# Performance work log

Measured on AMD Instinct MI355X. Metric: run time of the kernel, lower is better.

The kernel has to match this reference:

```python
import jax, jax.numpy as jnp
import numpy as np

B, LQ, LK, NF = 8, 8192, 1024, 64


def setup_inputs() -> dict:
    key = jax.random.key(0)
    k1, k2, k3, k4, k5 = jax.random.split(key, 5)
    x = jax.random.normal(k1, (B, LQ, NF), dtype=jnp.float32)
    kv = jax.random.normal(k2, (B, LK, NF), dtype=jnp.float32)
    # 1x1 submanifold convolutions == per-point linear maps (no bias)
    scale = 1.0 / np.sqrt(NF)
    Wq = jax.random.normal(k3, (NF, NF), dtype=jnp.float32) * scale
    Wk = jax.random.normal(k4, (NF, NF), dtype=jnp.float32) * scale
    Wv = jax.random.normal(k5, (NF, NF), dtype=jnp.float32) * scale
    return {"x": x, "kv": kv, "Wq": Wq, "Wk": Wk, "Wv": Wv}


def reference(x, kv, Wq, Wk, Wv):
    # q/k/v projections (1x1 convs on sparse features = dense matmuls)
    q = jnp.einsum("bqd,de->bqe", x, Wq)    # [B, LQ, NF]
    k = jnp.einsum("bkd,de->bke", kv, Wk)   # [B, LK, NF]
    v = jnp.einsum("bkd,de->bke", kv, Wv)   # [B, LK, NF]
    # per-batch (block-diagonal / ragged) attention: e = q k^T, softmax over keys, @ v
    scores = jnp.einsum("bqe,bke->bqk", q, k)        # [B, LQ, LK] (no scaling, as in source)
    attn = jax.nn.softmax(scores, axis=-1)
    out = jnp.einsum("bqk,bke->bqe", attn, v)        # [B, LQ, NF]
    return out
```

## Files before the change

kernel.cpp:

```cpp
#include <hip/hip_runtime.h>
#include <hip/hip_fp16.h>

constexpr int B_  = 8;
constexpr int LQ  = 8192;
constexpr int LK  = 1024;
constexpr int NF  = 64;
constexpr int PAD = 8;
constexpr int LDW = NF + PAD;

typedef _Float16 f16x8 __attribute__((ext_vector_type(8)));
typedef _Float16 f16x4 __attribute__((ext_vector_type(4)));
typedef float    f32x4 __attribute__((ext_vector_type(4)));

#define MFMA16(a, b, c) __builtin_amdgcn_mfma_f32_16x16x32_f16((a), (b), (c), 0, 0, 0)

__device__ __forceinline__ f16x8 cvt8(const float* p) {
  float4 a = ((const float4*)p)[0];
  float4 b = ((const float4*)p)[1];
  f16x8 r;
  r[0] = (_Float16)a.x; r[1] = (_Float16)a.y; r[2] = (_Float16)a.z; r[3] = (_Float16)a.w;
  r[4] = (_Float16)b.x; r[5] = (_Float16)b.y; r[6] = (_Float16)b.z; r[7] = (_Float16)b.w;
  return r;
}

__device__ __forceinline__ f16x8 ldf(const _Float16* p) { return *(const f16x8*)p; }

__device__ __forceinline__ void st_pk4(_Float16* dst, float a, float b, float c, float d) {
  auto lo = __builtin_amdgcn_cvt_pkrtz(a, b);
  auto hi = __builtin_amdgcn_cvt_pkrtz(c, d);
  auto v  = __builtin_shufflevector(lo, hi, 0, 1, 2, 3);
  *(decltype(v)*)dst = v;
}

__global__ __launch_bounds__(256) void kv_proj_kernel(
    const float* __restrict__ kv, const float* __restrict__ Wk,
    const float* __restrict__ Wv, _Float16* __restrict__ Kb,
    _Float16* __restrict__ Vt) {
  __shared__ __align__(16) _Float16 wkT[NF][LDW];
  __shared__ __align__(16) _Float16 wvT[NF][LDW];
  __shared__ __align__(16) _Float16 ktile[64][LDW];
  __shared__ __align__(16) _Float16 vtileT[64][LDW];

  const int t    = threadIdx.x;
  const int wave = t >> 6, lane = t & 63, g = lane >> 4, c = lane & 15;
  const int b    = blockIdx.x >> 4;
  const int key_base = (blockIdx.x & 15) * 64;

#pragma unroll
  for (int i = 0; i < 16; ++i) {
    int idx = t + 256 * i;
    int e = idx >> 6, d = idx & 63;
    wkT[d][e] = (_Float16)Wk[idx];
    wvT[d][e] = (_Float16)Wv[idx];
  }

  const float* src = kv + ((size_t)b * LK + key_base + wave * 16 + c) * NF;
  f16x8 a0 = cvt8(src + g * 8);
  f16x8 a1 = cvt8(src + 32 + g * 8);
  __syncthreads();

#pragma unroll
  for (int mb = 0; mb < 4; ++mb) {
    f32x4 kacc = {0.f, 0.f, 0.f, 0.f};
    const _Float16* wk0 = &wkT[mb * 16 + c][g * 8];
    kacc = MFMA16(ldf(wk0),      a0, kacc);
    kacc = MFMA16(ldf(wk0 + 32), a1, kacc);
    st_pk4(&ktile[wave * 16 + c][mb * 16 + g * 4], kacc[0], kacc[1], kacc[2], kacc[3]);

    f32x4 vacc = {0.f, 0.f, 0.f, 0.f};
    const _Float16* wv0 = &wvT[mb * 16 + c][g * 8];
    vacc = MFMA16(a0, ldf(wv0),      vacc);
    vacc = MFMA16(a1, ldf(wv0 + 32), vacc);
    st_pk4(&vtileT[mb * 16 + c][wave * 16 + g * 4], vacc[0], vacc[1], vacc[2], vacc[3]);
  }
  __syncthreads();

  const int srow = t >> 2, scol = (t & 3) * 16;
  {
    float4* kd = (float4*)(Kb + ((size_t)b * LK + key_base + srow) * NF + scol);
    kd[0] = *(float4*)&ktile[srow][scol];
    kd[1] = *(float4*)&ktile[srow][scol + 8];
    float4* vd = (float4*)(Vt + ((size_t)b * NF + srow) * LK + key_base + scol);
    vd[0] = *(float4*)&vtileT[srow][scol];
    vd[1] = *(float4*)&vtileT[srow][scol + 8];
  }
}

__global__ __launch_bounds__(256) void attn_kernel(
    const float* __restrict__ x, const float* __restrict__ Wq,
    const _Float16* __restrict__ Kb, const _Float16* __restrict__ Vt,
    float* __restrict__ out) {
  __shared__ __align__(16) _Float16 wqT[NF][LDW];
  __shared__ __align__(16) _Float16 ks[64][LDW];
  __shared__ __align__(16) _Float16 vs[64][LDW];
  __shared__ __align__(16) _Float16 ps[4][16][LDW];

  const int t    = threadIdx.x;
  const int wave = t >> 6, lane = t & 63, g = lane >> 4, c = lane & 15;
  const int b    = blockIdx.x >> 7;
  const int q_base = (blockIdx.x & 127) * 64;
  constexpr float LOG2E = 1.44269504088896f;

#pragma unroll
  for (int i = 0; i < 16; ++i) {
    int idx = t + 256 * i;
    wqT[idx & 63][idx >> 6] = (_Float16)(Wq[idx] * LOG2E);
  }

  const float* xrow = x + ((size_t)b * LQ + q_base + wave * 16 + c) * NF;
  f16x8 xa0 = cvt8(xrow + g * 8);
  f16x8 xa1 = cvt8(xrow + 32 + g * 8);

  const _Float16* Kg = Kb + (size_t)b * LK * NF;
  const _Float16* Vg = Vt + (size_t)b * NF * LK;
  const int srow = t >> 2, scol = (t & 3) * 16;

  float4 kp0, kp1, vp0, vp1;
  {
    const float4* kp = (const float4*)(Kg + (size_t)t * 16);
    kp0 = kp[0]; kp1 = kp[1];
    const float4* vp = (const float4*)(Vg + (size_t)srow * LK + scol);
    vp0 = vp[0]; vp1 = vp[1];
  }
  __syncthreads();

#pragma unroll
  for (int mb = 0; mb < 4; ++mb) {
    f32x4 qacc = {0.f, 0.f, 0.f, 0.f};
    const _Float16* wq0 = &wqT[mb * 16 + c][g * 8];
    qacc = MFMA16(ldf(wq0),      xa0, qacc);
    qacc = MFMA16(ldf(wq0 + 32), xa1, qacc);
    st_pk4(&ps[wave][c][mb * 16 + g * 4], qacc[0], qacc[1], qacc[2], qacc[3]);
  }
  f16x8 qb0 = ldf(&ps[wave][c][g * 8]);
  f16x8 qb1 = ldf(&ps[wave][c][32 + g * 8]);

  float m_s = -1e30f, l_s = 0.f;
  f32x4 oacc[4];
#pragma unroll
  for (int nb = 0; nb < 4; ++nb) oacc[nb] = {0.f, 0.f, 0.f, 0.f};

  for (int tile = 0; tile < 16; ++tile) {
    __syncthreads();
    *(f16x8*)&ks[srow][scol]     = *(f16x8*)&kp0;
    *(f16x8*)&ks[srow][scol + 8] = *(f16x8*)&kp1;
    *(f16x8*)&vs[srow][scol]     = *(f16x8*)&vp0;
    *(f16x8*)&vs[srow][scol + 8] = *(f16x8*)&vp1;
    __syncthreads();
    if (tile < 15) {
      const float4* kp = (const float4*)(Kg + (size_t)(tile + 1) * 64 * NF + t * 16);
      kp0 = kp[0]; kp1 = kp[1];
      const float4* vp = (const float4*)(Vg + (size_t)srow * LK + (tile + 1) * 64 + scol);
      vp0 = vp[0]; vp1 = vp[1];
    }

    f32x4 st[4];
#pragma unroll
    for (int kb = 0; kb < 4; ++kb) {
      st[kb] = {0.f, 0.f, 0.f, 0.f};
      const _Float16* kf = &ks[kb * 16 + c][g * 8];
      st[kb] = MFMA16(ldf(kf),      qb0, st[kb]);
      st[kb] = MFMA16(ldf(kf + 32), qb1, st[kb]);
    }

    float tmax = st[0][0];
#pragma unroll
    for (int kb = 0; kb < 4; ++kb)
#pragma unroll
      for (int r = 0; r < 4; ++r) tmax = fmaxf(tmax, st[kb][r]);
    tmax = fmaxf(tmax, __shfl_xor(tmax, 16));
    tmax = fmaxf(tmax, __shfl_xor(tmax, 32));

    float mnew  = fmaxf(m_s, tmax);
    float alpha = __builtin_amdgcn_exp2f(m_s - mnew);
    m_s = mnew;

    float rsum = 0.f;
#pragma unroll
    for (int kb = 0; kb < 4; ++kb)
#pragma unroll
      for (int r = 0; r < 4; ++r) {
        float p = __builtin_amdgcn_exp2f(st[kb][r] - mnew);
        st[kb][r] = p;
        rsum += p;
      }
    rsum += __shfl_xor(rsum, 16);
    rsum += __shfl_xor(rsum, 32);
    l_s = l_s * alpha + rsum;

    float aq[4];
#pragma unroll
    for (int r = 0; r < 4; ++r) aq[r] = __shfl(alpha, 4 * g + r);
#pragma unroll
    for (int nb = 0; nb < 4; ++nb)
#pragma unroll
      for (int r = 0; r < 4; ++r) oacc[nb][r] *= aq[r];

#pragma unroll
    for (int kb = 0; kb < 4; ++kb)
      st_pk4(&ps[wave][c][kb * 16 + g * 4], st[kb][0], st[kb][1], st[kb][2], st[kb][3]);
    f16x8 pa0 = ldf(&ps[wave][c][g * 8]);
    f16x8 pa1 = ldf(&ps[wave][c][32 + g * 8]);

#pragma unroll
    for (int nb = 0; nb < 4; ++nb) {
      const _Float16* vf = &vs[nb * 16 + c][g * 8];
      oacc[nb] = MFMA16(pa0, ldf(vf),      oacc[nb]);
      oacc[nb] = MFMA16(pa1, ldf(vf + 32), oacc[nb]);
    }
  }

  float linv = 1.0f / l_s;
  float lq[4];
#pragma unroll
  for (int r = 0; r < 4; ++r) lq[r] = __shfl(linv, 4 * g + r);
#pragma unroll
  for (int nb = 0; nb < 4; ++nb)
#pragma unroll
    for (int r = 0; r < 4; ++r)
      out[((size_t)b * LQ + q_base + wave * 16 + g * 4 + r) * NF + nb * 16 + c] =
          oacc[nb][r] * lq[r];
}

extern "C" void kernel_launch(void* const* d_in, const int* in_sizes, int n_in,
                              void* d_out, int out_size, void* d_ws, size_t ws_size,
                              hipStream_t stream) {
  const float* x  = (const float*)d_in[0];
  const float* kv = (const float*)d_in[1];
  const float* Wq = (const float*)d_in[2];
  const float* Wk = (const float*)d_in[3];
  const float* Wv = (const float*)d_in[4];
  float* out = (float*)d_out;

  _Float16* Kb = (_Float16*)d_ws;
  _Float16* Vt = Kb + (size_t)B_ * LK * NF;

  kv_proj_kernel<<<B_ * (LK / 64), 256, 0, stream>>>(kv, Wk, Wv, Kb, Vt);
  attn_kernel<<<B_ * (LQ / 64), 256, 0, stream>>>(x, Wq, Kb, Vt, out);
}
```

Baseline: 114.0 us.

## Process two query sub-tiles per wave and keep softmax probabilities in registers

The attention kernel drops to 128 threads per block, with each wave handling 32 query rows as two 16-row sub-tiles. Each K and V fragment read from LDS now feeds twice as many MFMAs. K and V are stored pre-permuted by the projection kernel, so Q and the probabilities P are packed straight from MFMA accumulators into operand registers, removing the LDS round trip through ps. A ballot skips the output rescale when the running max does not change, and Wq staging reuses the K tile buffer. The cost is higher register pressure from doubled accumulators, V loads that are no longer prefetched, and fewer threads to hide latency.

```diff
diff --git a/kernel.cpp b/kernel.cpp
--- a/kernel.cpp
+++ b/kernel.cpp
@@ -9,7 +9,6 @@
 constexpr int LDW = NF + PAD;
 
 typedef _Float16 f16x8 __attribute__((ext_vector_type(8)));
-typedef _Float16 f16x4 __attribute__((ext_vector_type(4)));
 typedef float    f32x4 __attribute__((ext_vector_type(4)));
 
 #define MFMA16(a, b, c) __builtin_amdgcn_mfma_f32_16x16x32_f16((a), (b), (c), 0, 0, 0)
@@ -30,6 +29,17 @@
   auto hi = __builtin_amdgcn_cvt_pkrtz(c, d);
   auto v  = __builtin_shufflevector(lo, hi, 0, 1, 2, 3);
   *(decltype(v)*)dst = v;
+}
+
+__device__ __forceinline__ f16x8 pack8(f32x4 u, f32x4 v) {
+  auto a = __builtin_amdgcn_cvt_pkrtz(u[0], u[1]);
+  auto b = __builtin_amdgcn_cvt_pkrtz(u[2], u[3]);
+  auto cc = __builtin_amdgcn_cvt_pkrtz(v[0], v[1]);
+  auto d = __builtin_amdgcn_cvt_pkrtz(v[2], v[3]);
+  f16x8 r;
+  r[0] = a[0]; r[1] = a[1]; r[2] = b[0];  r[3] = b[1];
+  r[4] = cc[0]; r[5] = cc[1]; r[6] = d[0]; r[7] = d[1];
+  return r;
 }
 
 __global__ __launch_bounds__(256) void kv_proj_kernel(
@@ -65,13 +75,15 @@
     const _Float16* wk0 = &wkT[mb * 16 + c][g * 8];
     kacc = MFMA16(ldf(wk0),      a0, kacc);
     kacc = MFMA16(ldf(wk0 + 32), a1, kacc);
-    st_pk4(&ktile[wave * 16 + c][mb * 16 + g * 4], kacc[0], kacc[1], kacc[2], kacc[3]);
+    st_pk4(&ktile[wave * 16 + c][(8 * (mb >> 1) + 2 * g + (mb & 1)) * 4],
+           kacc[0], kacc[1], kacc[2], kacc[3]);
 
     f32x4 vacc = {0.f, 0.f, 0.f, 0.f};
     const _Float16* wv0 = &wvT[mb * 16 + c][g * 8];
     vacc = MFMA16(a0, ldf(wv0),      vacc);
     vacc = MFMA16(a1, ldf(wv0 + 32), vacc);
-    st_pk4(&vtileT[mb * 16 + c][wave * 16 + g * 4], vacc[0], vacc[1], vacc[2], vacc[3]);
+    st_pk4(&vtileT[mb * 16 + c][(8 * (wave >> 1) + 2 * g + (wave & 1)) * 4],
+           vacc[0], vacc[1], vacc[2], vacc[3]);
   }
   __syncthreads();
 
@@ -86,14 +98,12 @@
   }
 }
 
-__global__ __launch_bounds__(256) void attn_kernel(
+__global__ __launch_bounds__(128, 4) void attn_kernel(
     const float* __restrict__ x, const float* __restrict__ Wq,
     const _Float16* __restrict__ Kb, const _Float16* __restrict__ Vt,
     float* __restrict__ out) {
-  __shared__ __align__(16) _Float16 wqT[NF][LDW];
   __shared__ __align__(16) _Float16 ks[64][LDW];
   __shared__ __align__(16) _Float16 vs[64][LDW];
-  __shared__ __align__(16) _Float16 ps[4][16][LDW];
 
   const int t    = threadIdx.x;
   const int wave = t >> 6, lane = t & 63, g = lane >> 4, c = lane & 15;
@@ -102,124 +112,147 @@
   constexpr float LOG2E = 1.44269504088896f;
 
 #pragma unroll
-  for (int i = 0; i < 16; ++i) {
-    int idx = t + 256 * i;
-    wqT[idx & 63][idx >> 6] = (_Float16)(Wq[idx] * LOG2E);
-  }
-
-  const float* xrow = x + ((size_t)b * LQ + q_base + wave * 16 + c) * NF;
-  f16x8 xa0 = cvt8(xrow + g * 8);
-  f16x8 xa1 = cvt8(xrow + 32 + g * 8);
+  for (int i = 0; i < 32; ++i) {
+    int idx = t + 128 * i;
+    ks[idx & 63][idx >> 6] = (_Float16)(Wq[idx] * LOG2E);
+  }
 
   const _Float16* Kg = Kb + (size_t)b * LK * NF;
   const _Float16* Vg = Vt + (size_t)b * NF * LK;
-  const int srow = t >> 2, scol = (t & 3) * 16;
-
-  float4 kp0, kp1, vp0, vp1;
+  const int srow = t >> 1, shalf = t & 1;
+
+  f16x8 kpre[4];
   {
-    const float4* kp = (const float4*)(Kg + (size_t)t * 16);
-    kp0 = kp[0]; kp1 = kp[1];
-    const float4* vp = (const float4*)(Vg + (size_t)srow * LK + scol);
-    vp0 = vp[0]; vp1 = vp[1];
-  }
-  __syncthreads();
-
-#pragma unroll
-  for (int mb = 0; mb < 4; ++mb) {
-    f32x4 qacc = {0.f, 0.f, 0.f, 0.f};
-    const _Float16* wq0 = &wqT[mb * 16 + c][g * 8];
-    qacc = MFMA16(ldf(wq0),      xa0, qacc);
-    qacc = MFMA16(ldf(wq0 + 32), xa1, qacc);
-    st_pk4(&ps[wave][c][mb * 16 + g * 4], qacc[0], qacc[1], qacc[2], qacc[3]);
-  }
-  f16x8 qb0 = ldf(&ps[wave][c][g * 8]);
-  f16x8 qb1 = ldf(&ps[wave][c][32 + g * 8]);
-
-  float m_s = -1e30f, l_s = 0.f;
-  f32x4 oacc[4];
-#pragma unroll
-  for (int nb = 0; nb < 4; ++nb) oacc[nb] = {0.f, 0.f, 0.f, 0.f};
+    const f16x8* kp = (const f16x8*)(Kg + srow * NF + shalf * 32);
+    kpre[0] = kp[0]; kpre[1] = kp[1]; kpre[2] = kp[2]; kpre[3] = kp[3];
+  }
+  __syncthreads();
+
+  f16x8 qb[2][2];
+#pragma unroll
+  for (int s = 0; s < 2; ++s) {
+    const float* xrow = x + ((size_t)b * LQ + q_base + wave * 32 + s * 16 + c) * NF;
+    f16x8 xa0 = cvt8(xrow + g * 8);
+    f16x8 xa1 = cvt8(xrow + 32 + g * 8);
+    f32x4 qa[4];
+#pragma unroll
+    for (int mb = 0; mb < 4; ++mb) {
+      qa[mb] = {0.f, 0.f, 0.f, 0.f};
+      const _Float16* wq0 = &ks[mb * 16 + c][g * 8];
+      qa[mb] = MFMA16(ldf(wq0),      xa0, qa[mb]);
+      qa[mb] = MFMA16(ldf(wq0 + 32), xa1, qa[mb]);
+    }
+    qb[s][0] = pack8(qa[0], qa[1]);
+    qb[s][1] = pack8(qa[2], qa[3]);
+  }
+  __syncthreads();
+
+  float m_s[2] = {-1e30f, -1e30f}, l_s[2] = {0.f, 0.f};
+  f32x4 oacc[2][4];
+#pragma unroll
+  for (int s = 0; s < 2; ++s)
+#pragma unroll
+    for (int nb = 0; nb < 4; ++nb) oacc[s][nb] = {0.f, 0.f, 0.f, 0.f};
 
   for (int tile = 0; tile < 16; ++tile) {
-    __syncthreads();
-    *(f16x8*)&ks[srow][scol]     = *(f16x8*)&kp0;
-    *(f16x8*)&ks[srow][scol + 8] = *(f16x8*)&kp1;
-    *(f16x8*)&vs[srow][scol]     = *(f16x8*)&vp0;
-    *(f16x8*)&vs[srow][scol + 8] = *(f16x8*)&vp1;
+    *(f16x8*)&ks[srow][shalf * 32]      = kpre[0];
+    *(f16x8*)&ks[srow][shalf * 32 + 8]  = kpre[1];
+    *(f16x8*)&ks[srow][shalf * 32 + 16] = kpre[2];
+    *(f16x8*)&ks[srow][shalf * 32 + 24] = kpre[3];
+    {
+      const f16x8* vp = (const f16x8*)(Vg + (size_t)srow * LK + tile * 64 + shalf * 32);
+      f16x8 v0 = vp[0], v1 = vp[1], v2 = vp[2], v3 = vp[3];
+      *(f16x8*)&vs[srow][shalf * 32]      = v0;
+      *(f16x8*)&vs[srow][shalf * 32 + 8]  = v1;
+      *(f16x8*)&vs[srow][shalf * 32 + 16] = v2;
+      *(f16x8*)&vs[srow][shalf * 32 + 24] = v3;
+    }
     __syncthreads();
     if (tile < 15) {
-      const float4* kp = (const float4*)(Kg + (size_t)(tile + 1) * 64 * NF + t * 16);
-      kp0 = kp[0]; kp1 = kp[1];
-      const float4* vp = (const float4*)(Vg + (size_t)srow * LK + (tile + 1) * 64 + scol);
-      vp0 = vp[0]; vp1 = vp[1];
-    }
-
-    f32x4 st[4];
+      const f16x8* kp = (const f16x8*)(Kg + (size_t)(tile + 1) * 64 * NF + srow * NF + shalf * 32);
+      kpre[0] = kp[0]; kpre[1] = kp[1]; kpre[2] = kp[2]; kpre[3] = kp[3];
+    }
+
+    f32x4 st[2][4];
 #pragma unroll
     for (int kb = 0; kb < 4; ++kb) {
-      st[kb] = {0.f, 0.f, 0.f, 0.f};
       const _Float16* kf = &ks[kb * 16 + c][g * 8];
-      st[kb] = MFMA16(ldf(kf),      qb0, st[kb]);
-      st[kb] = MFMA16(ldf(kf + 32), qb1, st[kb]);
-    }
-
-    float tmax = st[0][0];
-#pragma unroll
-    for (int kb = 0; kb < 4; ++kb)
-#pragma unroll
-      for (int r = 0; r < 4; ++r) tmax = fmaxf(tmax, st[kb][r]);
-    tmax = fmaxf(tmax, __shfl_xor(tmax, 16));
-    tmax = fmaxf(tmax, __shfl_xor(tmax, 32));
-
-    float mnew  = fmaxf(m_s, tmax);
-    float alpha = __builtin_amdgcn_exp2f(m_s - mnew);
-    m_s = mnew;
-
-    float rsum = 0.f;
-#pragma unroll
-    for (int kb = 0; kb < 4; ++kb)
-#pragma unroll
-      for (int r = 0; r < 4; ++r) {
-        float p = __builtin_amdgcn_exp2f(st[kb][r] - mnew);
-        st[kb][r] = p;
-        rsum += p;
+      f16x8 k0 = ldf(kf), k1 = ldf(kf + 32);
+      st[0][kb] = {0.f, 0.f, 0.f, 0.f};
+      st[1][kb] = {0.f, 0.f, 0.f, 0.f};
+      st[0][kb] = MFMA16(k0, qb[0][0], st[0][kb]);
+      st[0][kb] = MFMA16(k1, qb[0][1], st[0][kb]);
+      st[1][kb] = MFMA16(k0, qb[1][0], st[1][kb]);
+      st[1][kb] = MFMA16(k1, qb[1][1], st[1][kb]);
+    }
+
+    f16x8 pa[2][2];
+#pragma unroll
+    for (int s = 0; s < 2; ++s) {
+      float tmax = st[s][0][0];
+#pragma unroll
+      for (int kb = 0; kb < 4; ++kb)
+#pragma unroll
+        for (int r = 0; r < 4; ++r) tmax = fmaxf(tmax, st[s][kb][r]);
+      tmax = fmaxf(tmax, __shfl_xor(tmax, 16));
+      tmax = fmaxf(tmax, __shfl_xor(tmax, 32));
+
+      if (__ballot(tmax > m_s[s]) != 0) {
+        float mnew  = fmaxf(m_s[s], tmax);
+        float alpha = __builtin_amdgcn_exp2f(m_s[s] - mnew);
+        m_s[s] = mnew;
+        l_s[s] *= alpha;
+        float aq[4];
+#pragma unroll
+        for (int r = 0; r < 4; ++r) aq[r] = __shfl(alpha, 4 * g + r);
+#pragma unroll
+        for (int nb = 0; nb < 4; ++nb)
+#pragma unroll
+          for (int r = 0; r < 4; ++r) oacc[s][nb][r] *= aq[r];
       }
-    rsum += __shfl_xor(rsum, 16);
-    rsum += __shfl_xor(rsum, 32);
-    l_s = l_s * alpha + rsum;
-
-    float aq[4];
-#pragma unroll
-    for (int r = 0; r < 4; ++r) aq[r] = __shfl(alpha, 4 * g + r);
-#pragma unroll
-    for (int nb = 0; nb < 4; ++nb)
-#pragma unroll
-      for (int r = 0; r < 4; ++r) oacc[nb][r] *= aq[r];
-
-#pragma unroll
-    for (int kb = 0; kb < 4; ++kb)
-      st_pk4(&ps[wave][c][kb * 16 + g * 4], st[kb][0], st[kb][1], st[kb][2], st[kb][3]);
-    f16x8 pa0 = ldf(&ps[wave][c][g * 8]);
-    f16x8 pa1 = ldf(&ps[wave][c][32 + g * 8]);
+
+      float rsum = 0.f;
+#pragma unroll
+      for (int kb = 0; kb < 4; ++kb)
+#pragma unroll
+        for (int r = 0; r < 4; ++r) {
+          float p = __builtin_amdgcn_exp2f(st[s][kb][r] - m_s[s]);
+          st[s][kb][r] = p;
+          rsum += p;
+        }
+      rsum += __shfl_xor(rsum, 16);
+      rsum += __shfl_xor(rsum, 32);
+      l_s[s] += rsum;
+
+      pa[s][0] = pack8(st[s][0], st[s][1]);
+      pa[s][1] = pack8(st[s][2], st[s][3]);
+    }
 
 #pragma unroll
     for (int nb = 0; nb < 4; ++nb) {
       const _Float16* vf = &vs[nb * 16 + c][g * 8];
-      oacc[nb] = MFMA16(pa0, ldf(vf),      oacc[nb]);
-      oacc[nb] = MFMA16(pa1, ldf(vf + 32), oacc[nb]);
-    }
-  }
-
-  float linv = 1.0f / l_s;
-  float lq[4];
-#pragma unroll
-  for (int r = 0; r < 4; ++r) lq[r] = __shfl(linv, 4 * g + r);
-#pragma unroll
-  for (int nb = 0; nb < 4; ++nb)
-#pragma unroll
-    for (int r = 0; r < 4; ++r)
-      out[((size_t)b * LQ + q_base + wave * 16 + g * 4 + r) * NF + nb * 16 + c] =
-          oacc[nb][r] * lq[r];
+      f16x8 v0 = ldf(vf), v1 = ldf(vf + 32);
+      oacc[0][nb] = MFMA16(pa[0][0], v0, oacc[0][nb]);
+      oacc[0][nb] = MFMA16(pa[0][1], v1, oacc[0][nb]);
+      oacc[1][nb] = MFMA16(pa[1][0], v0, oacc[1][nb]);
+      oacc[1][nb] = MFMA16(pa[1][1], v1, oacc[1][nb]);
+    }
+    __syncthreads();
+  }
+
+#pragma unroll
+  for (int s = 0; s < 2; ++s) {
+    float linv = 1.0f / l_s[s];
+    float lq[4];
+#pragma unroll
+    for (int r = 0; r < 4; ++r) lq[r] = __shfl(linv, 4 * g + r);
+#pragma unroll
+    for (int nb = 0; nb < 4; ++nb)
+#pragma unroll
+      for (int r = 0; r < 4; ++r)
+        out[((size_t)b * LQ + q_base + wave * 32 + s * 16 + 4 * g + r) * NF + nb * 16 + c] =
+            oacc[s][nb][r] * lq[r];
+  }
 }
 
 extern "C" void kernel_launch(void* const* d_in, const int* in_sizes, int n_in,
@@ -236,5 +269,5 @@
   _Float16* Vt = Kb + (size_t)B_ * LK * NF;
 
   kv_proj_kernel<<<B_ * (LK / 64), 256, 0, stream>>>(kv, Wk, Wv, Kb, Vt);
-  attn_kernel<<<B_ * (LQ / 64), 256, 0, stream>>>(x, Wq, Kb, Vt, out);
-}
+  attn_kernel<<<B_ * (LQ / 64), 128, 0, stream>>>(x, Wq, Kb, Vt, out);
+}
```

New measurement: 110.6 us. 2.9% less time.
